# Kernel optimization log

Hardware: AMD Instinct MI355X
Metric: run time of the kernel (lower is better)

The kernel has to match this reference:

```python
import jax, jax.numpy as jnp
import numpy as np

B, D_IN, D_H = 262144, 128, 128
PROJ_EPS = 1e-5  # ball projection epsilon (c = 1.0)


def _norm(x):
    return jnp.linalg.norm(x, axis=-1, keepdims=True)


def logmap0(x):
    # atanh(||x||) * x / ||x||, safe at 0 (c = 1)
    n = _norm(x)
    ns = jnp.where(n == 0, 0.5, n)
    return jnp.where(n == 0, jnp.zeros_like(x), jnp.arctanh(ns) * x / ns)


def expmap0(v):
    # tanh(||v||) * v / ||v||, safe at 0 (c = 1)
    n = _norm(v)
    ns = jnp.where(n == 0, 1.0, n)
    return jnp.where(n == 0, jnp.zeros_like(v), jnp.tanh(ns) * v / ns)


def proj(x):
    # clip back inside the unit Poincare ball
    n = _norm(x)
    maxnorm = 1.0 - PROJ_EPS
    ns = jnp.where(n == 0, 1.0, n)
    return jnp.where(n > maxnorm, x / ns * maxnorm, x)


def setup_inputs() -> dict:
    key = jax.random.key(0)
    ks = jax.random.split(key, 8)
    scale = 0.03  # keep points well inside the ball: ||x|| ~ 0.03*sqrt(128) ~ 0.34
    x = scale * jax.random.normal(ks[0], (B, D_IN), dtype=jnp.float32)
    h = scale * jax.random.normal(ks[1], (B, D_H), dtype=jnp.float32)
    fan_in = D_IN + D_H
    w_std = 1.0 / np.sqrt(fan_in)
    Wr = w_std * jax.random.normal(ks[2], (fan_in, D_H), dtype=jnp.float32)
    br = w_std * jax.random.normal(ks[3], (D_H,), dtype=jnp.float32)
    Wz = w_std * jax.random.normal(ks[4], (fan_in, D_H), dtype=jnp.float32)
    bz = w_std * jax.random.normal(ks[5], (D_H,), dtype=jnp.float32)
    Wh = w_std * jax.random.normal(ks[6], (fan_in, D_H), dtype=jnp.float32)
    bh = w_std * jax.random.normal(ks[7], (D_H,), dtype=jnp.float32)
    return {"x": x, "h": h, "Wr": Wr, "br": br, "Wz": Wz, "bz": bz, "Wh": Wh, "bh": bh}


def reference(x, h, Wr, br, Wz, bz, Wh, bh):
    x_tan = logmap0(x)            # [B, D_IN]
    h_tan = logmap0(h)            # [B, D_H]
    xh = jnp.concatenate([x_tan, h_tan], axis=1)  # [B, D_IN+D_H]
    r = jax.nn.sigmoid(xh @ Wr + br)
    z = jax.nn.sigmoid(xh @ Wz + bz)
    xh_reset = jnp.concatenate([x_tan, r * h_tan], axis=1)
    h_tilde = jnp.tanh(xh_reset @ Wh + bh)
    h_new_tan = (1.0 - z) * h_tan + z * h_tilde
    return proj(expmap0(h_new_tan))  # [B, D_H]
```

## Files before the change

### kernel.cpp

```cpp
#include <hip/hip_runtime.h>
#include <hip/hip_bf16.h>

typedef __attribute__((ext_vector_type(4))) float f32x4;
typedef __attribute__((ext_vector_type(8))) short bf16x8;
typedef __attribute__((ext_vector_type(4))) short bf16x4;
typedef __attribute__((ext_vector_type(2))) unsigned int u32x2;

#define D 128
#define BM 32

__device__ __forceinline__ unsigned short f2bf(float f){
  union { float f; unsigned int i; } c; c.f = f;
  unsigned int i = c.i;
  i += 0x7fffu + ((i >> 16) & 1u);
  return (unsigned short)(i >> 16);
}
__device__ __forceinline__ float bf2f(unsigned short u){
  union { float f; unsigned int i; } c; c.i = ((unsigned int)u) << 16; return c.f;
}
__device__ __forceinline__ unsigned int pk2(float a, float b){
  __hip_bfloat162 t = __float22bfloat162_rn(make_float2(a, b));
  return *reinterpret_cast<unsigned int*>(&t);
}
__device__ __forceinline__ float rcp_f(float x){ return __builtin_amdgcn_rcpf(x); }
__device__ __forceinline__ float exp2_f(float x){ return __builtin_amdgcn_exp2f(x); }
__device__ __forceinline__ float sigmoid_f(float t){
  return rcp_f(1.0f + exp2_f(-1.442695041f * t));
}
__device__ __forceinline__ float tanh_f(float t){
  return __builtin_fmaf(2.0f, rcp_f(1.0f + exp2_f(-2.885390082f * t)), -1.0f);
}

__global__ void prep_weights(const float* __restrict__ Wr, const float* __restrict__ Wz,
                             const float* __restrict__ Wh, unsigned short* __restrict__ wp)
{
  int w = blockIdx.x >> 6;
  int f = blockIdx.x & 63;
  int l = threadIdx.x;
  const float* src = (w == 0) ? Wr : ((w == 1) ? Wz : Wh);
  int nf = f >> 3, kk = f & 7;
  int col = nf * 16 + (l & 15);
  int k0  = kk * 32 + (l >> 4) * 8;
  unsigned short* dst = wp + w * 32768 + (f * 64 + l) * 8;
#pragma unroll
  for (int j = 0; j < 8; ++j)
    dst[j] = f2bf(src[(k0 + j) * D + col]);
}

__global__ __launch_bounds__(256, 5) void gru_fused(
    const float* __restrict__ x, const float* __restrict__ h,
    const float* __restrict__ brp, const float* __restrict__ bzp, const float* __restrict__ bhp,
    const unsigned short* __restrict__ wp, float* __restrict__ out)
{
  __shared__ __align__(16) unsigned char A1[BM * 512];
  float* P = (float*)A1;

  const int tid = threadIdx.x;
  const int w   = tid >> 6;
  const int l   = tid & 63;
  const int l15 = l & 15;
  const int lq  = l >> 4;
  const size_t row0 = (size_t)blockIdx.x * BM;

  {
    const int row = tid >> 3;
    const int q   = tid & 7;
    const f32x4* xr = (const f32x4*)(x + (row0 + row) * D);
    const f32x4* hr = (const f32x4*)(h + (row0 + row) * D);
    f32x4 v[4];
    float ss = 0.f;
#pragma unroll
    for (int j = 0; j < 4; ++j){
      v[j] = xr[j * 8 + q];
      ss += v[j][0]*v[j][0] + v[j][1]*v[j][1] + v[j][2]*v[j][2] + v[j][3]*v[j][3];
    }
    ss += __shfl_xor(ss, 1, 64);
    ss += __shfl_xor(ss, 2, 64);
    ss += __shfl_xor(ss, 4, 64);
    float n = __builtin_amdgcn_sqrtf(ss);
    float s = 1.f;
    if (n > 1e-20f)
      s = 0.34657359f * __builtin_amdgcn_logf((1.f + n) * rcp_f(1.f - n)) * rcp_f(n);
#pragma unroll
    for (int j = 0; j < 4; ++j){
      unsigned int byte = (unsigned)(row * 512 + (8 * j + q) * 8) ^ (unsigned)((row & 7) << 4);
      u32x2 pk; pk[0] = pk2(v[j][0] * s, v[j][1] * s); pk[1] = pk2(v[j][2] * s, v[j][3] * s);
      *(u32x2*)(A1 + byte) = pk;
    }
    ss = 0.f;
#pragma unroll
    for (int j = 0; j < 4; ++j){
      v[j] = hr[j * 8 + q];
      ss += v[j][0]*v[j][0] + v[j][1]*v[j][1] + v[j][2]*v[j][2] + v[j][3]*v[j][3];
    }
    ss += __shfl_xor(ss, 1, 64);
    ss += __shfl_xor(ss, 2, 64);
    ss += __shfl_xor(ss, 4, 64);
    n = __builtin_amdgcn_sqrtf(ss);
    s = 1.f;
    if (n > 1e-20f)
      s = 0.34657359f * __builtin_amdgcn_logf((1.f + n) * rcp_f(1.f - n)) * rcp_f(n);
#pragma unroll
    for (int j = 0; j < 4; ++j){
      unsigned int byte = (unsigned)(row * 512 + 256 + (8 * j + q) * 8) ^ (unsigned)((row & 7) << 4);
      u32x2 pk; pk[0] = pk2(v[j][0] * s, v[j][1] * s); pk[1] = pk2(v[j][2] * s, v[j][3] * s);
      *(u32x2*)(A1 + byte) = pk;
    }
  }
  __syncthreads();

  const unsigned short* pwr = wp + w * 8192;
  const unsigned short* pwz = wp + 32768 + w * 8192;

  f32x4 ar0[2], ar1[2], az0[2], az1[2];
#pragma unroll
  for (int m = 0; m < 2; ++m){ ar0[m] = 0; ar1[m] = 0; az0[m] = 0; az1[m] = 0; }

#pragma unroll 2
  for (int kk = 0; kk < 8; ++kk){
    const bf16x8 wr0 = *(const bf16x8*)(pwr + kk * 512 + l * 8);
    const bf16x8 wr1 = *(const bf16x8*)(pwr + 4096 + kk * 512 + l * 8);
    const bf16x8 wz0 = *(const bf16x8*)(pwz + kk * 512 + l * 8);
    const bf16x8 wz1 = *(const bf16x8*)(pwz + 4096 + kk * 512 + l * 8);
#pragma unroll
    for (int m = 0; m < 2; ++m){
      const int row = m * 16 + l15;
      unsigned int byte = (unsigned)(row * 512 + (kk * 32 + lq * 8) * 2) ^ (unsigned)((row & 7) << 4);
      const bf16x8 b = *(const bf16x8*)(A1 + byte);
      ar0[m] = __builtin_amdgcn_mfma_f32_16x16x32_bf16(wr0, b, ar0[m], 0, 0, 0);
      ar1[m] = __builtin_amdgcn_mfma_f32_16x16x32_bf16(wr1, b, ar1[m], 0, 0, 0);
      az0[m] = __builtin_amdgcn_mfma_f32_16x16x32_bf16(wz0, b, az0[m], 0, 0, 0);
      az1[m] = __builtin_amdgcn_mfma_f32_16x16x32_bf16(wz1, b, az1[m], 0, 0, 0);
    }
  }

  const int c00 = w * 32 + lq * 4;
  const int c01 = c00 + 16;
  const f32x4 brv0 = *(const f32x4*)(brp + c00);
  const f32x4 brv1 = *(const f32x4*)(brp + c01);
  const f32x4 bzv0 = *(const f32x4*)(bzp + c00);
  const f32x4 bzv1 = *(const f32x4*)(bzp + c01);

  f32x4 zk0[2], zk1[2];
  u32x2 htp0[2], htp1[2];
  u32x2 rhp0[2], rhp1[2];
#pragma unroll
  for (int m = 0; m < 2; ++m){
    const int row = m * 16 + l15;
    const unsigned int swz = (unsigned)((row & 7) << 4);
    const bf16x4 h40 = *(const bf16x4*)(A1 + ((unsigned)(row * 512 + (128 + c00) * 2) ^ swz));
    const bf16x4 h41 = *(const bf16x4*)(A1 + ((unsigned)(row * 512 + (128 + c01) * 2) ^ swz));
    htp0[m] = *(const u32x2*)&h40;
    htp1[m] = *(const u32x2*)&h41;
    float rh0[4], rh1[4];
#pragma unroll
    for (int reg = 0; reg < 4; ++reg){
      float r0 = sigmoid_f(ar0[m][reg] + brv0[reg]);
      float r1 = sigmoid_f(ar1[m][reg] + brv1[reg]);
      zk0[m][reg] = sigmoid_f(az0[m][reg] + bzv0[reg]);
      zk1[m][reg] = sigmoid_f(az1[m][reg] + bzv1[reg]);
      rh0[reg] = r0 * bf2f((unsigned short)h40[reg]);
      rh1[reg] = r1 * bf2f((unsigned short)h41[reg]);
    }
    rhp0[m][0] = pk2(rh0[0], rh0[1]); rhp0[m][1] = pk2(rh0[2], rh0[3]);
    rhp1[m][0] = pk2(rh1[0], rh1[1]); rhp1[m][1] = pk2(rh1[2], rh1[3]);
  }
  __syncthreads();

#pragma unroll
  for (int m = 0; m < 2; ++m){
    const int row = m * 16 + l15;
    const unsigned int swz = (unsigned)((row & 7) << 4);
    *(u32x2*)(A1 + ((unsigned)(row * 512 + (128 + c00) * 2) ^ swz)) = rhp0[m];
    *(u32x2*)(A1 + ((unsigned)(row * 512 + (128 + c01) * 2) ^ swz)) = rhp1[m];
  }
  __syncthreads();

  const unsigned short* pwh = wp + 65536 + w * 8192;
  f32x4 ah0[2], ah1[2];
#pragma unroll
  for (int m = 0; m < 2; ++m){ ah0[m] = 0; ah1[m] = 0; }

#pragma unroll 2
  for (int kk = 0; kk < 8; ++kk){
    const bf16x8 wh0 = *(const bf16x8*)(pwh + kk * 512 + l * 8);
    const bf16x8 wh1 = *(const bf16x8*)(pwh + 4096 + kk * 512 + l * 8);
#pragma unroll
    for (int m = 0; m < 2; ++m){
      const int row = m * 16 + l15;
      unsigned int byte = (unsigned)(row * 512 + (kk * 32 + lq * 8) * 2) ^ (unsigned)((row & 7) << 4);
      const bf16x8 b = *(const bf16x8*)(A1 + byte);
      ah0[m] = __builtin_amdgcn_mfma_f32_16x16x32_bf16(wh0, b, ah0[m], 0, 0, 0);
      ah1[m] = __builtin_amdgcn_mfma_f32_16x16x32_bf16(wh1, b, ah1[m], 0, 0, 0);
    }
  }

  const f32x4 bhv0 = *(const f32x4*)(bhp + c00);
  const f32x4 bhv1 = *(const f32x4*)(bhp + c01);
  f32x4 o0[2], o1[2];
#pragma unroll
  for (int m = 0; m < 2; ++m){
#pragma unroll
    for (int reg = 0; reg < 4; ++reg){
      float htld0 = tanh_f(ah0[m][reg] + bhv0[reg]);
      float htld1 = tanh_f(ah1[m][reg] + bhv1[reg]);
      float ht0 = bf2f((unsigned short)(htp0[m][reg >> 1] >> ((reg & 1) * 16)));
      float ht1 = bf2f((unsigned short)(htp1[m][reg >> 1] >> ((reg & 1) * 16)));
      float z0 = zk0[m][reg], z1 = zk1[m][reg];
      o0[m][reg] = (1.f - z0) * ht0 + z0 * htld0;
      o1[m][reg] = (1.f - z1) * ht1 + z1 * htld1;
    }
  }
  __syncthreads();

#pragma unroll
  for (int m = 0; m < 2; ++m){
    const int row = m * 16 + l15;
    float s = 0.f;
#pragma unroll
    for (int reg = 0; reg < 4; ++reg)
      s += o0[m][reg]*o0[m][reg] + o1[m][reg]*o1[m][reg];
    s += __shfl_xor(s, 16, 64);
    s += __shfl_xor(s, 32, 64);
    if (lq == 0) P[row * 4 + w] = s;
  }
  __syncthreads();

#pragma unroll
  for (int m = 0; m < 2; ++m){
    const int row = m * 16 + l15;
    const f32x4 p4 = *(const f32x4*)(P + row * 4);
    float ss = p4[0] + p4[1] + p4[2] + p4[3];
    float n = __builtin_amdgcn_sqrtf(ss);
    float sc = 1.f;
    if (n > 1e-20f){
      float th = tanh_f(n);
      th = fminf(th, 0.99999f);
      sc = th * rcp_f(n);
    }
    float* orow = out + (row0 + row) * D;
    f32x4 st0 = o0[m] * sc;
    f32x4 st1 = o1[m] * sc;
    *(f32x4*)(orow + c00) = st0;
    *(f32x4*)(orow + c01) = st1;
  }
}

extern "C" void kernel_launch(void* const* d_in, const int* in_sizes, int n_in,
                              void* d_out, int out_size, void* d_ws, size_t ws_size,
                              hipStream_t stream)
{
  const float* x   = (const float*)d_in[0];
  const float* h   = (const float*)d_in[1];
  const float* Wr  = (const float*)d_in[2];
  const float* brp = (const float*)d_in[3];
  const float* Wz  = (const float*)d_in[4];
  const float* bzp = (const float*)d_in[5];
  const float* Wh  = (const float*)d_in[6];
  const float* bhp = (const float*)d_in[7];
  unsigned short* wsp = (unsigned short*)d_ws;

  prep_weights<<<192, 64, 0, stream>>>(Wr, Wz, Wh, wsp);
  gru_fused<<<262144 / BM, 256, 0, stream>>>(x, h, brp, bzp, bhp, wsp, (float*)d_out);
}
```

Before: 134.3 us.

## Process multiple row tiles per block with async global-to-LDS prefetch of inputs

```diff
diff --git a/kernel.cpp b/kernel.cpp
--- a/kernel.cpp
+++ b/kernel.cpp
@@ -5,9 +5,12 @@
 typedef __attribute__((ext_vector_type(8))) short bf16x8;
 typedef __attribute__((ext_vector_type(4))) short bf16x4;
 typedef __attribute__((ext_vector_type(2))) unsigned int u32x2;
+typedef const __attribute__((address_space(1))) unsigned int g_u32;
+typedef __attribute__((address_space(3))) unsigned int l_u32;
 
 #define D 128
 #define BM 32
+#define TILES 4
 
 __device__ __forceinline__ unsigned short f2bf(float f){
   union { float f; unsigned int i; } c; c.f = f;
@@ -47,202 +50,229 @@
     dst[j] = f2bf(src[(k0 + j) * D + col]);
 }
 
-__global__ __launch_bounds__(256, 5) void gru_fused(
+__device__ __forceinline__ void stage_tile(const float* gx, const float* gh,
+                                           unsigned char* Sx, unsigned char* Sh,
+                                           int w, int l)
+{
+#pragma unroll
+  for (int c2 = 0; c2 < 4; ++c2){
+    const unsigned off = (unsigned)(c2 * 4096 + w * 1024);
+    __builtin_amdgcn_global_load_lds(
+        (g_u32*)(const void*)((const unsigned char*)gx + off + l * 16),
+        (l_u32*)(void*)(Sx + off), 16, 0, 0);
+    __builtin_amdgcn_global_load_lds(
+        (g_u32*)(const void*)((const unsigned char*)gh + off + l * 16),
+        (l_u32*)(void*)(Sh + off), 16, 0, 0);
+  }
+}
+
+__global__ __launch_bounds__(256, 3) void gru_fused(
     const float* __restrict__ x, const float* __restrict__ h,
     const float* __restrict__ brp, const float* __restrict__ bzp, const float* __restrict__ bhp,
     const unsigned short* __restrict__ wp, float* __restrict__ out)
 {
   __shared__ __align__(16) unsigned char A1[BM * 512];
-  float* P = (float*)A1;
+  __shared__ __align__(16) unsigned char Sx[BM * 512];
+  __shared__ __align__(16) unsigned char Sh[BM * 512];
+  __shared__ float P[BM * 4];
 
   const int tid = threadIdx.x;
   const int w   = tid >> 6;
   const int l   = tid & 63;
   const int l15 = l & 15;
   const int lq  = l >> 4;
-  const size_t row0 = (size_t)blockIdx.x * BM;
-
-  {
-    const int row = tid >> 3;
-    const int q   = tid & 7;
-    const f32x4* xr = (const f32x4*)(x + (row0 + row) * D);
-    const f32x4* hr = (const f32x4*)(h + (row0 + row) * D);
-    f32x4 v[4];
-    float ss = 0.f;
-#pragma unroll
-    for (int j = 0; j < 4; ++j){
-      v[j] = xr[j * 8 + q];
-      ss += v[j][0]*v[j][0] + v[j][1]*v[j][1] + v[j][2]*v[j][2] + v[j][3]*v[j][3];
-    }
-    ss += __shfl_xor(ss, 1, 64);
-    ss += __shfl_xor(ss, 2, 64);
-    ss += __shfl_xor(ss, 4, 64);
-    float n = __builtin_amdgcn_sqrtf(ss);
-    float s = 1.f;
-    if (n > 1e-20f)
-      s = 0.34657359f * __builtin_amdgcn_logf((1.f + n) * rcp_f(1.f - n)) * rcp_f(n);
-#pragma unroll
-    for (int j = 0; j < 4; ++j){
-      unsigned int byte = (unsigned)(row * 512 + (8 * j + q) * 8) ^ (unsigned)((row & 7) << 4);
-      u32x2 pk; pk[0] = pk2(v[j][0] * s, v[j][1] * s); pk[1] = pk2(v[j][2] * s, v[j][3] * s);
-      *(u32x2*)(A1 + byte) = pk;
-    }
-    ss = 0.f;
-#pragma unroll
-    for (int j = 0; j < 4; ++j){
-      v[j] = hr[j * 8 + q];
-      ss += v[j][0]*v[j][0] + v[j][1]*v[j][1] + v[j][2]*v[j][2] + v[j][3]*v[j][3];
-    }
-    ss += __shfl_xor(ss, 1, 64);
-    ss += __shfl_xor(ss, 2, 64);
-    ss += __shfl_xor(ss, 4, 64);
-    n = __builtin_amdgcn_sqrtf(ss);
-    s = 1.f;
-    if (n > 1e-20f)
-      s = 0.34657359f * __builtin_amdgcn_logf((1.f + n) * rcp_f(1.f - n)) * rcp_f(n);
-#pragma unroll
-    for (int j = 0; j < 4; ++j){
-      unsigned int byte = (unsigned)(row * 512 + 256 + (8 * j + q) * 8) ^ (unsigned)((row & 7) << 4);
-      u32x2 pk; pk[0] = pk2(v[j][0] * s, v[j][1] * s); pk[1] = pk2(v[j][2] * s, v[j][3] * s);
-      *(u32x2*)(A1 + byte) = pk;
-    }
-  }
-  __syncthreads();
 
   const unsigned short* pwr = wp + w * 8192;
   const unsigned short* pwz = wp + 32768 + w * 8192;
-
-  f32x4 ar0[2], ar1[2], az0[2], az1[2];
-#pragma unroll
-  for (int m = 0; m < 2; ++m){ ar0[m] = 0; ar1[m] = 0; az0[m] = 0; az1[m] = 0; }
+  const unsigned short* pwh = wp + 65536 + w * 8192;
+
+  const size_t tile0 = (size_t)blockIdx.x * TILES;
+
+  stage_tile(x + tile0 * BM * D, h + tile0 * BM * D, Sx, Sh, w, l);
+  __syncthreads();
+
+  for (int k = 0; k < TILES; ++k){
+    const size_t row0 = (tile0 + k) * BM;
+
+    {
+      const int prow = tid >> 3;
+      const int q    = tid & 7;
+      const int c    = (q + prow) & 7;
+      const unsigned swzw = (unsigned)((prow & 7) << 4);
+      int fo[4];
+#pragma unroll
+      for (int j = 0; j < 4; ++j)
+        fo[j] = c * 16 + ((((prow & 3) + j) & 3) << 2);
+
+      f32x4 v[4];
+      float ss = 0.f;
+#pragma unroll
+      for (int j = 0; j < 4; ++j){
+        v[j] = *(const f32x4*)(Sx + prow * 512 + fo[j] * 4);
+        ss += v[j][0]*v[j][0] + v[j][1]*v[j][1] + v[j][2]*v[j][2] + v[j][3]*v[j][3];
+      }
+      ss += __shfl_xor(ss, 1, 64);
+      ss += __shfl_xor(ss, 2, 64);
+      ss += __shfl_xor(ss, 4, 64);
+      float n = __builtin_amdgcn_sqrtf(ss);
+      float s = 1.f;
+      if (n > 1e-20f)
+        s = 0.34657359f * __builtin_amdgcn_logf((1.f + n) * rcp_f(1.f - n)) * rcp_f(n);
+#pragma unroll
+      for (int j = 0; j < 4; ++j){
+        u32x2 pk; pk[0] = pk2(v[j][0] * s, v[j][1] * s); pk[1] = pk2(v[j][2] * s, v[j][3] * s);
+        *(u32x2*)(A1 + ((unsigned)(prow * 512 + fo[j] * 2) ^ swzw)) = pk;
+      }
+      ss = 0.f;
+#pragma unroll
+      for (int j = 0; j < 4; ++j){
+        v[j] = *(const f32x4*)(Sh + prow * 512 + fo[j] * 4);
+        ss += v[j][0]*v[j][0] + v[j][1]*v[j][1] + v[j][2]*v[j][2] + v[j][3]*v[j][3];
+      }
+      ss += __shfl_xor(ss, 1, 64);
+      ss += __shfl_xor(ss, 2, 64);
+      ss += __shfl_xor(ss, 4, 64);
+      n = __builtin_amdgcn_sqrtf(ss);
+      s = 1.f;
+      if (n > 1e-20f)
+        s = 0.34657359f * __builtin_amdgcn_logf((1.f + n) * rcp_f(1.f - n)) * rcp_f(n);
+#pragma unroll
+      for (int j = 0; j < 4; ++j){
+        u32x2 pk; pk[0] = pk2(v[j][0] * s, v[j][1] * s); pk[1] = pk2(v[j][2] * s, v[j][3] * s);
+        *(u32x2*)(A1 + ((unsigned)(prow * 512 + 256 + fo[j] * 2) ^ swzw)) = pk;
+      }
+    }
+    __syncthreads();
+
+    if (k + 1 < TILES)
+      stage_tile(x + (row0 + BM) * D, h + (row0 + BM) * D, Sx, Sh, w, l);
+
+    f32x4 ar0[2], ar1[2], az0[2], az1[2];
+#pragma unroll
+    for (int m = 0; m < 2; ++m){ ar0[m] = 0; ar1[m] = 0; az0[m] = 0; az1[m] = 0; }
 
 #pragma unroll 2
-  for (int kk = 0; kk < 8; ++kk){
-    const bf16x8 wr0 = *(const bf16x8*)(pwr + kk * 512 + l * 8);
-    const bf16x8 wr1 = *(const bf16x8*)(pwr + 4096 + kk * 512 + l * 8);
-    const bf16x8 wz0 = *(const bf16x8*)(pwz + kk * 512 + l * 8);
-    const bf16x8 wz1 = *(const bf16x8*)(pwz + 4096 + kk * 512 + l * 8);
-#pragma unroll
-    for (int m = 0; m < 2; ++m){
-      const int row = m * 16 + l15;
-      unsigned int byte = (unsigned)(row * 512 + (kk * 32 + lq * 8) * 2) ^ (unsigned)((row & 7) << 4);
-      const bf16x8 b = *(const bf16x8*)(A1 + byte);
-      ar0[m] = __builtin_amdgcn_mfma_f32_16x16x32_bf16(wr0, b, ar0[m], 0, 0, 0);
-      ar1[m] = __builtin_amdgcn_mfma_f32_16x16x32_bf16(wr1, b, ar1[m], 0, 0, 0);
-      az0[m] = __builtin_amdgcn_mfma_f32_16x16x32_bf16(wz0, b, az0[m], 0, 0, 0);
-      az1[m] = __builtin_amdgcn_mfma_f32_16x16x32_bf16(wz1, b, az1[m], 0, 0, 0);
-    }
-  }
-
-  const int c00 = w * 32 + lq * 4;
-  const int c01 = c00 + 16;
-  const f32x4 brv0 = *(const f32x4*)(brp + c00);
-  const f32x4 brv1 = *(const f32x4*)(brp + c01);
-  const f32x4 bzv0 = *(const f32x4*)(bzp + c00);
-  const f32x4 bzv1 = *(const f32x4*)(bzp + c01);
-
-  f32x4 zk0[2], zk1[2];
-  u32x2 htp0[2], htp1[2];
-  u32x2 rhp0[2], rhp1[2];
-#pragma unroll
-  for (int m = 0; m < 2; ++m){
-    const int row = m * 16 + l15;
-    const unsigned int swz = (unsigned)((row & 7) << 4);
-    const bf16x4 h40 = *(const bf16x4*)(A1 + ((unsigned)(row * 512 + (128 + c00) * 2) ^ swz));
-    const bf16x4 h41 = *(const bf16x4*)(A1 + ((unsigned)(row * 512 + (128 + c01) * 2) ^ swz));
-    htp0[m] = *(const u32x2*)&h40;
-    htp1[m] = *(const u32x2*)&h41;
-    float rh0[4], rh1[4];
-#pragma unroll
-    for (int reg = 0; reg < 4; ++reg){
-      float r0 = sigmoid_f(ar0[m][reg] + brv0[reg]);
-      float r1 = sigmoid_f(ar1[m][reg] + brv1[reg]);
-      zk0[m][reg] = sigmoid_f(az0[m][reg] + bzv0[reg]);
-      zk1[m][reg] = sigmoid_f(az1[m][reg] + bzv1[reg]);
-      rh0[reg] = r0 * bf2f((unsigned short)h40[reg]);
-      rh1[reg] = r1 * bf2f((unsigned short)h41[reg]);
-    }
-    rhp0[m][0] = pk2(rh0[0], rh0[1]); rhp0[m][1] = pk2(rh0[2], rh0[3]);
-    rhp1[m][0] = pk2(rh1[0], rh1[1]); rhp1[m][1] = pk2(rh1[2], rh1[3]);
-  }
-  __syncthreads();
-
-#pragma unroll
-  for (int m = 0; m < 2; ++m){
-    const int row = m * 16 + l15;
-    const unsigned int swz = (unsigned)((row & 7) << 4);
-    *(u32x2*)(A1 + ((unsigned)(row * 512 + (128 + c00) * 2) ^ swz)) = rhp0[m];
-    *(u32x2*)(A1 + ((unsigned)(row * 512 + (128 + c01) * 2) ^ swz)) = rhp1[m];
-  }
-  __syncthreads();
-
-  const unsigned short* pwh = wp + 65536 + w * 8192;
-  f32x4 ah0[2], ah1[2];
-#pragma unroll
-  for (int m = 0; m < 2; ++m){ ah0[m] = 0; ah1[m] = 0; }
+    for (int kk = 0; kk < 8; ++kk){
+      const bf16x8 wr0 = *(const bf16x8*)(pwr + kk * 512 + l * 8);
+      const bf16x8 wr1 = *(const bf16x8*)(pwr + 4096 + kk * 512 + l * 8);
+      const bf16x8 wz0 = *(const bf16x8*)(pwz + kk * 512 + l * 8);
+      const bf16x8 wz1 = *(const bf16x8*)(pwz + 4096 + kk * 512 + l * 8);
+#pragma unroll
+      for (int m = 0; m < 2; ++m){
+        const int row = m * 16 + l15;
+        unsigned int byte = (unsigned)(row * 512 + (kk * 32 + lq * 8) * 2) ^ (unsigned)((row & 7) << 4);
+        const bf16x8 b = *(const bf16x8*)(A1 + byte);
+        ar0[m] = __builtin_amdgcn_mfma_f32_16x16x32_bf16(wr0, b, ar0[m], 0, 0, 0);
+        ar1[m] = __builtin_amdgcn_mfma_f32_16x16x32_bf16(wr1, b, ar1[m], 0, 0, 0);
+        az0[m] = __builtin_amdgcn_mfma_f32_16x16x32_bf16(wz0, b, az0[m], 0, 0, 0);
+        az1[m] = __builtin_amdgcn_mfma_f32_16x16x32_bf16(wz1, b, az1[m], 0, 0, 0);
+      }
+    }
+
+    const int c00 = w * 32 + lq * 4;
+    const int c01 = c00 + 16;
+    const f32x4 brv0 = *(const f32x4*)(brp + c00);
+    const f32x4 brv1 = *(const f32x4*)(brp + c01);
+    const f32x4 bzv0 = *(const f32x4*)(bzp + c00);
+    const f32x4 bzv1 = *(const f32x4*)(bzp + c01);
+
+    f32x4 zk0[2], zk1[2];
+    u32x2 htp0[2], htp1[2];
+    u32x2 rhp0[2], rhp1[2];
+#pragma unroll
+    for (int m = 0; m < 2; ++m){
+      const int row = m * 16 + l15;
+      const unsigned int swz = (unsigned)((row & 7) << 4);
+      const bf16x4 h40 = *(const bf16x4*)(A1 + ((unsigned)(row * 512 + (128 + c00) * 2) ^ swz));
+      const bf16x4 h41 = *(const bf16x4*)(A1 + ((unsigned)(row * 512 + (128 + c01) * 2) ^ swz));
+      htp0[m] = *(const u32x2*)&h40;
+      htp1[m] = *(const u32x2*)&h41;
+      float rh0[4], rh1[4];
+#pragma unroll
+      for (int reg = 0; reg < 4; ++reg){
+        float r0 = sigmoid_f(ar0[m][reg] + brv0[reg]);
+        float r1 = sigmoid_f(ar1[m][reg] + brv1[reg]);
+        zk0[m][reg] = sigmoid_f(az0[m][reg] + bzv0[reg]);
+        zk1[m][reg] = sigmoid_f(az1[m][reg] + bzv1[reg]);
+        rh0[reg] = r0 * bf2f((unsigned short)h40[reg]);
+        rh1[reg] = r1 * bf2f((unsigned short)h41[reg]);
+      }
+      rhp0[m][0] = pk2(rh0[0], rh0[1]); rhp0[m][1] = pk2(rh0[2], rh0[3]);
+      rhp1[m][0] = pk2(rh1[0], rh1[1]); rhp1[m][1] = pk2(rh1[2], rh1[3]);
+    }
+    __syncthreads();
+
+#pragma unroll
+    for (int m = 0; m < 2; ++m){
+      const int row = m * 16 + l15;
+      const unsigned int swz = (unsigned)((row & 7) << 4);
+      *(u32x2*)(A1 + ((unsigned)(row * 512 + (128 + c00) * 2) ^ swz)) = rhp0[m];
+      *(u32x2*)(A1 + ((unsigned)(row * 512 + (128 + c01) * 2) ^ swz)) = rhp1[m];
+    }
+    __syncthreads();
+
+    f32x4 ah0[2], ah1[2];
+#pragma unroll
+    for (int m = 0; m < 2; ++m){ ah0[m] = 0; ah1[m] = 0; }
 
 #pragma unroll 2
-  for (int kk = 0; kk < 8; ++kk){
-    const bf16x8 wh0 = *(const bf16x8*)(pwh + kk * 512 + l * 8);
-    const bf16x8 wh1 = *(const bf16x8*)(pwh + 4096 + kk * 512 + l * 8);
-#pragma unroll
-    for (int m = 0; m < 2; ++m){
-      const int row = m * 16 + l15;
-      unsigned int byte = (unsigned)(row * 512 + (kk * 32 + lq * 8) * 2) ^ (unsigned)((row & 7) << 4);
-      const bf16x8 b = *(const bf16x8*)(A1 + byte);
-      ah0[m] = __builtin_amdgcn_mfma_f32_16x16x32_bf16(wh0, b, ah0[m], 0, 0, 0);
-      ah1[m] = __builtin_amdgcn_mfma_f32_16x16x32_bf16(wh1, b, ah1[m], 0, 0, 0);
-    }
-  }
-
-  const f32x4 bhv0 = *(const f32x4*)(bhp + c00);
-  const f32x4 bhv1 = *(const f32x4*)(bhp + c01);
-  f32x4 o0[2], o1[2];
-#pragma unroll
-  for (int m = 0; m < 2; ++m){
-#pragma unroll
-    for (int reg = 0; reg < 4; ++reg){
-      float htld0 = tanh_f(ah0[m][reg] + bhv0[reg]);
-      float htld1 = tanh_f(ah1[m][reg] + bhv1[reg]);
-      float ht0 = bf2f((unsigned short)(htp0[m][reg >> 1] >> ((reg & 1) * 16)));
-      float ht1 = bf2f((unsigned short)(htp1[m][reg >> 1] >> ((reg & 1) * 16)));
-      float z0 = zk0[m][reg], z1 = zk1[m][reg];
-      o0[m][reg] = (1.f - z0) * ht0 + z0 * htld0;
-      o1[m][reg] = (1.f - z1) * ht1 + z1 * htld1;
-    }
-  }
-  __syncthreads();
-
-#pragma unroll
-  for (int m = 0; m < 2; ++m){
-    const int row = m * 16 + l15;
-    float s = 0.f;
-#pragma unroll
-    for (int reg = 0; reg < 4; ++reg)
-      s += o0[m][reg]*o0[m][reg] + o1[m][reg]*o1[m][reg];
-    s += __shfl_xor(s, 16, 64);
-    s += __shfl_xor(s, 32, 64);
-    if (lq == 0) P[row * 4 + w] = s;
-  }
-  __syncthreads();
-
-#pragma unroll
-  for (int m = 0; m < 2; ++m){
-    const int row = m * 16 + l15;
-    const f32x4 p4 = *(const f32x4*)(P + row * 4);
-    float ss = p4[0] + p4[1] + p4[2] + p4[3];
-    float n = __builtin_amdgcn_sqrtf(ss);
-    float sc = 1.f;
-    if (n > 1e-20f){
-      float th = tanh_f(n);
-      th = fminf(th, 0.99999f);
-      sc = th * rcp_f(n);
-    }
-    float* orow = out + (row0 + row) * D;
-    f32x4 st0 = o0[m] * sc;
-    f32x4 st1 = o1[m] * sc;
-    *(f32x4*)(orow + c00) = st0;
-    *(f32x4*)(orow + c01) = st1;
+    for (int kk = 0; kk < 8; ++kk){
+      const bf16x8 wh0 = *(const bf16x8*)(pwh + kk * 512 + l * 8);
+      const bf16x8 wh1 = *(const bf16x8*)(pwh + 4096 + kk * 512 + l * 8);
+#pragma unroll
+      for (int m = 0; m < 2; ++m){
+        const int row = m * 16 + l15;
+        unsigned int byte = (unsigned)(row * 512 + (kk * 32 + lq * 8) * 2) ^ (unsigned)((row & 7) << 4);
+        const bf16x8 b = *(const bf16x8*)(A1 + byte);
+        ah0[m] = __builtin_amdgcn_mfma_f32_16x16x32_bf16(wh0, b, ah0[m], 0, 0, 0);
+        ah1[m] = __builtin_amdgcn_mfma_f32_16x16x32_bf16(wh1, b, ah1[m], 0, 0, 0);
+      }
+    }
+
+    const f32x4 bhv0 = *(const f32x4*)(bhp + c00);
+    const f32x4 bhv1 = *(const f32x4*)(bhp + c01);
+    f32x4 o0[2], o1[2];
+#pragma unroll
+    for (int m = 0; m < 2; ++m){
+#pragma unroll
+      for (int reg = 0; reg < 4; ++reg){
+        float htld0 = tanh_f(ah0[m][reg] + bhv0[reg]);
+        float htld1 = tanh_f(ah1[m][reg] + bhv1[reg]);
+        float ht0 = bf2f((unsigned short)(htp0[m][reg >> 1] >> ((reg & 1) * 16)));
+        float ht1 = bf2f((unsigned short)(htp1[m][reg >> 1] >> ((reg & 1) * 16)));
+        float z0 = zk0[m][reg], z1 = zk1[m][reg];
+        o0[m][reg] = ht0 + z0 * (htld0 - ht0);
+        o1[m][reg] = ht1 + z1 * (htld1 - ht1);
+      }
+      const int row = m * 16 + l15;
+      float s = 0.f;
+#pragma unroll
+      for (int reg = 0; reg < 4; ++reg)
+        s += o0[m][reg]*o0[m][reg] + o1[m][reg]*o1[m][reg];
+      s += __shfl_xor(s, 16, 64);
+      s += __shfl_xor(s, 32, 64);
+      if (lq == 0) P[row * 4 + w] = s;
+    }
+    __syncthreads();
+
+#pragma unroll
+    for (int m = 0; m < 2; ++m){
+      const int row = m * 16 + l15;
+      const f32x4 p4 = *(const f32x4*)(P + row * 4);
+      float ss = p4[0] + p4[1] + p4[2] + p4[3];
+      float n = __builtin_amdgcn_sqrtf(ss);
+      float sc = 1.f;
+      if (n > 1e-20f){
+        float th = tanh_f(n);
+        th = fminf(th, 0.99999f);
+        sc = th * rcp_f(n);
+      }
+      float* orow = out + (row0 + row) * D;
+      f32x4 st0 = o0[m] * sc;
+      f32x4 st1 = o1[m] * sc;
+      *(f32x4*)(orow + c00) = st0;
+      *(f32x4*)(orow + c01) = st1;
+    }
   }
 }
 
@@ -261,5 +291,5 @@
   unsigned short* wsp = (unsigned short*)d_ws;
 
   prep_weights<<<192, 64, 0, stream>>>(Wr, Wz, Wh, wsp);
-  gru_fused<<<262144 / BM, 256, 0, stream>>>(x, h, brp, bzp, bhp, wsp, (float*)d_out);
-}
+  gru_fused<<<262144 / (BM * TILES), 256, 0, stream>>>(x, h, brp, bzp, bhp, wsp, (float*)d_out);
+}
```

Measured after the change: 138.8 us. +3.4%, slower.
